# Kernel tuning notes

Hardware: AMD Instinct MI355X
Metric: run time of the kernel (lower is better)

Reference implementation:

```python
import jax, jax.numpy as jnp
import numpy as np

EPS = 1e-3  # Keras BatchNormalization default epsilon


def _bn_params(key, c):
    k1, k2, k3, k4 = jax.random.split(key, 4)
    gamma = 1.0 + 0.1 * jax.random.normal(k1, (c,), jnp.float32)
    beta = 0.1 * jax.random.normal(k2, (c,), jnp.float32)
    mean = 0.1 * jax.random.normal(k3, (c,), jnp.float32)
    var = 0.5 + jax.random.uniform(k4, (c,), jnp.float32)
    return jnp.stack([gamma, beta, mean, var])  # (4, c)


def bn(x, p):
    g, b, m, v = p[0], p[1], p[2], p[3]
    return (x - m) * jax.lax.rsqrt(v + EPS) * g + b


def setup_inputs() -> dict:
    key = jax.random.key(0)
    ks = jax.random.split(key, 32)
    B, N, C, K = 32, 2048, 3, 32
    MLP1, UNITS = 128, 512
    w = lambda k, shp, fan: jax.random.normal(k, shp, jnp.float32) / np.sqrt(fan)
    inp = {
        "inputs": jax.random.normal(ks[0], (B, N, C), jnp.float32),
        "indices": jax.random.randint(ks[1], (B, N, K), 0, N, jnp.int32),
        "t_conv1_w": w(ks[2], (C, 64), C), "t_conv1_b": 0.1 * jax.random.normal(ks[3], (64,), jnp.float32),
        "t_bn1": _bn_params(ks[4], 64),
        "t_dense1_w": w(ks[5], (64, 64), 64), "t_dense1_b": 0.1 * jax.random.normal(ks[6], (64,), jnp.float32),
        "t_bn2": _bn_params(ks[7], 64),
        "t_dense2_w": w(ks[8], (64, C * C), 64), "t_dense2_b": 0.1 * jax.random.normal(ks[9], (C * C,), jnp.float32),
        "conv1_w": w(ks[10], (K * C, MLP1), K * C), "conv1_b": 0.1 * jax.random.normal(ks[11], (MLP1,), jnp.float32),
        "bn1": _bn_params(ks[12], MLP1),
        "conv2_w": w(ks[13], (MLP1, 2 * MLP1), MLP1), "conv2_b": 0.1 * jax.random.normal(ks[14], (2 * MLP1,), jnp.float32),
        "bn2": _bn_params(ks[15], 2 * MLP1),
        "bn3": _bn_params(ks[16], 2 * MLP1),
        "dense1_w": w(ks[17], (2 * MLP1, C), 2 * MLP1), "dense1_b": 0.1 * jax.random.normal(ks[18], (C,), jnp.float32),
        "conv3_w": w(ks[19], (C, UNITS), C), "conv3_b": 0.1 * jax.random.normal(ks[20], (UNITS,), jnp.float32),
        "bn4": _bn_params(ks[21], UNITS),
        "blk1_w": w(ks[22], (UNITS, UNITS // 2), UNITS), "blk1_b": 0.1 * jax.random.normal(ks[23], (UNITS // 2,), jnp.float32),
        "blk1_bn": _bn_params(ks[24], UNITS // 2),
        "blk2_w": w(ks[25], (UNITS // 2, UNITS // 4), UNITS // 2), "blk2_b": 0.1 * jax.random.normal(ks[26], (UNITS // 4,), jnp.float32),
        "blk2_bn": _bn_params(ks[27], UNITS // 4),
        "bn_globf": _bn_params(ks[28], UNITS // 4),
    }
    return inp


def reference(inputs, indices, t_conv1_w, t_conv1_b, t_bn1, t_dense1_w, t_dense1_b,
              t_bn2, t_dense2_w, t_dense2_b, conv1_w, conv1_b, bn1, conv2_w, conv2_b,
              bn2, bn3, dense1_w, dense1_b, conv3_w, conv3_b, bn4,
              blk1_w, blk1_b, blk1_bn, blk2_w, blk2_b, blk2_bn, bn_globf):
    B, N, C = inputs.shape
    # --- TNetLess (inference: dropout = identity) ---
    x = jax.nn.relu(bn(inputs @ t_conv1_w + t_conv1_b, t_bn1))   # (B,N,64)
    x = jnp.max(x, axis=1)                                        # global max pool -> (B,64)
    x = jax.nn.relu(bn(x @ t_dense1_w + t_dense1_b, t_bn2))      # (B,64)
    transform = (x @ t_dense2_w + t_dense2_b).reshape(B, C, C)   # (B,C,C)
    pct = jnp.einsum('bnc,bcd->bnd', inputs, transform)          # transformed cloud (B,N,C)
    # --- random neighbor gather (batch_dims=1) ---
    feats = pct[jnp.arange(B)[:, None, None], indices]           # (B,N,K,C)
    feats = feats.reshape(B, N, -1)                               # (B,N,K*C)
    # --- pointwise MLP over gathered neighbor features ---
    feats = jax.nn.relu(bn(feats @ conv1_w + conv1_b, bn1))      # (B,N,128)
    feats = jax.nn.relu(bn(feats @ conv2_w + conv2_b, bn2))      # (B,N,256)
    g = bn(jnp.max(feats, axis=1), bn3)                           # (B,256)
    g = jnp.broadcast_to(g[:, None, :], (B, N, g.shape[-1]))     # tile to (B,N,256)
    g = g @ dense1_w + dense1_b                                   # (B,N,C)
    combined = jnp.concatenate([pct, g], axis=1)                  # concat on point axis -> (B,2N,C)
    # --- conv3 + conv blocks (kernel_size=1 -> pointwise) ---
    net = jax.nn.relu(bn(combined @ conv3_w + conv3_b, bn4))     # (B,2N,512)
    net = jax.nn.relu(bn(net @ blk1_w + blk1_b, blk1_bn))        # (B,2N,256)
    net = jax.nn.relu(bn(net @ blk2_w + blk2_b, blk2_bn))        # (B,2N,128)
    net = jnp.max(net, axis=1)                                    # (B,128)
    return bn(net, bn_globf)
```

## Files before the change

### kernel.cpp

```cpp
#include <hip/hip_runtime.h>

typedef unsigned short u16;
typedef unsigned int u32;
typedef __attribute__((ext_vector_type(8))) short bf16x8;
typedef __attribute__((ext_vector_type(4))) float f32x4;

#define EPSBN 0.001f
#define MFMA16(a, b, c) __builtin_amdgcn_mfma_f32_16x16x32_bf16(a, b, c, 0, 0, 0)

__device__ __forceinline__ float bf2f(u16 u) {
    return __uint_as_float(((u32)u) << 16);
}
__device__ __forceinline__ u16 f2bf(float f) {
    u32 u = __float_as_uint(f);
    u32 r = u + 0x7FFFu + ((u >> 16) & 1u);
    return (u16)(r >> 16);
}
__device__ __forceinline__ float relu(float x) { return x > 0.f ? x : 0.f; }

#define A_INPUTS 64
#define A_TC1W  196672
#define A_TC1B  196864
#define A_TBN1  196928
#define A_TD1W  197184
#define A_TD1B  201280
#define A_TBN2  201344
#define A_TD2W  201600
#define A_TD2B  202176
#define A_C1W   202240
#define A_C1B   214528
#define A_BN1   214656
#define A_C2W   215168
#define A_C2B   247936
#define A_BN2   248192
#define A_BN3   249216
#define A_D1W   250240
#define A_D1B   251008
#define A_C3W   251072
#define A_C3B   252608
#define A_BN4   253120
#define A_BLK1W 255168
#define A_BLK1B 386240
#define A_BLK1BN 386496
#define A_BLK2W 387520
#define A_BLK2B 420288
#define A_BLK2BN 420416
#define A_BNGF  420928
#define S_TRF   423488
#define S_PCT   423808
#define S_MAXF  620544
#define S_NETMAX 628736
#define S_XMAX  632832
#define T_C1WT  634880
#define T_C2WT  641024
#define T_W4T   657408
#define T_W5T   722944
#define P_W3S   739328
#define P_B3S   740864
#define P_BP1   741376
#define P_BP2   741504
#define P_BP4   741760
#define P_BP5   742016

struct ConvArgs {
    const void* src[28];
    int n[28];
    int off[28];
};

struct PrepArgs {
    const float* src[4];
    const float* bn[4];
    u16* dst[4];
    int K[4];
    int logN[4];
    int base[4];
};

__global__ __launch_bounds__(256) void k_convert(ConvArgs a, const u16* __restrict__ tbn1,
                                                 float* __restrict__ ws, u32* __restrict__ flag) {
    int ok = 1;
    for (int i = 0; i < 16; i += 2) {
        u16 v = tbn1[i];
        if (v < 0x3E00u || v > 0x4080u) ok = 0;
    }
    if (blockIdx.x == 0 && blockIdx.y == 0 && threadIdx.x == 0) flag[0] = ok ? 1u : 0u;

    int t = blockIdx.y;
    int n = a.n[t];
    int cpb = (n + 31) >> 5;
    int s = blockIdx.x * cpb;
    int e = s + cpb; if (e > n) e = n;
    float* dst = ws + a.off[t];
    if (ok) {
        const u16* src = (const u16*)a.src[t];
        for (int i = s + (int)threadIdx.x; i < e; i += 256) dst[i] = bf2f(src[i]);
    } else {
        const float* src = (const float*)a.src[t];
        for (int i = s + (int)threadIdx.x; i < e; i += 256) dst[i] = src[i];
    }
}

__global__ __launch_bounds__(256) void k_prepw_all(PrepArgs pa) {
    int blk = blockIdx.x;
    int t = (blk < 48) ? 0 : (blk < 176) ? 1 : (blk < 688) ? 2 : 3;
    int i = (blk - pa.base[t]) * 256 + (int)threadIdx.x;
    int N = 1 << pa.logN[t];
    int k = i >> pa.logN[t], c = i & (N - 1);
    const float* bn = pa.bn[t];
    float s = bn[c] * rsqrtf(bn[3 * N + c] + EPSBN);
    pa.dst[t][c * pa.K[t] + k] = f2bf(pa.src[t][i] * s);
}

__global__ __launch_bounds__(256) void k_prepsmall(float* __restrict__ ws) {
    int tid = threadIdx.x;
    for (int c = tid; c < 512; c += 256) {
        const float* bn = ws + A_BN4;
        float s = bn[c] * rsqrtf(bn[1536 + c] + EPSBN);
        float t = bn[512 + c] - bn[1024 + c] * s;
        ws[P_W3S + c]        = ws[A_C3W + c] * s;
        ws[P_W3S + 512 + c]  = ws[A_C3W + 512 + c] * s;
        ws[P_W3S + 1024 + c] = ws[A_C3W + 1024 + c] * s;
        ws[P_B3S + c] = ws[A_C3B + c] * s + t;
    }
    {
        int c = tid;
        const float* bn2 = ws + A_BN2;
        float s2 = bn2[c] * rsqrtf(bn2[768 + c] + EPSBN);
        ws[P_BP2 + c] = ws[A_C2B + c] * s2 + (bn2[256 + c] - bn2[512 + c] * s2);
        const float* bn5 = ws + A_BLK1BN;
        float s5 = bn5[c] * rsqrtf(bn5[768 + c] + EPSBN);
        ws[P_BP4 + c] = ws[A_BLK1B + c] * s5 + (bn5[256 + c] - bn5[512 + c] * s5);
    }
    if (tid < 128) {
        int c = tid;
        const float* bn1 = ws + A_BN1;
        float s1 = bn1[c] * rsqrtf(bn1[384 + c] + EPSBN);
        ws[P_BP1 + c] = ws[A_C1B + c] * s1 + (bn1[128 + c] - bn1[256 + c] * s1);
        const float* bn6 = ws + A_BLK2BN;
        float s6 = bn6[c] * rsqrtf(bn6[384 + c] + EPSBN);
        ws[P_BP5 + c] = ws[A_BLK2B + c] * s6 + (bn6[128 + c] - bn6[256 + c] * s6);
    }
}

__global__ __launch_bounds__(256) void k_tnet1(const float* __restrict__ inp,
                                               const float* __restrict__ w,
                                               const float* __restrict__ bias,
                                               const float* __restrict__ bn,
                                               u32* __restrict__ xmax) {
    __shared__ float pts[1536];
    __shared__ float wred[4][64];
    int b = blockIdx.y, slice = blockIdx.x, tid = threadIdx.x;
    const float* ip = inp + ((size_t)b * 2048 + slice * 512) * 3;
#pragma unroll
    for (int i = 0; i < 6; i++) pts[tid + i * 256] = ip[tid + i * 256];

    int c = tid & 63, np = tid >> 6;
    float w0 = w[c], w1 = w[64 + c], w2 = w[128 + c], bi = bias[c];
    float g = bn[c], be = bn[64 + c], m = bn[128 + c], v = bn[192 + c];
    float s = g * rsqrtf(v + EPSBN), t = be - m * s;
    __syncthreads();

    float vmax = 0.f;
    int pbase = np * 128;
#pragma unroll 4
    for (int p = 0; p < 128; p++) {
        float x0 = pts[(pbase + p) * 3], x1 = pts[(pbase + p) * 3 + 1], x2 = pts[(pbase + p) * 3 + 2];
        float z = x0 * w0 + x1 * w1 + x2 * w2 + bi;
        vmax = fmaxf(vmax, z * s + t);
    }
    wred[np][c] = vmax;
    __syncthreads();
    if (tid < 64) {
        float mm = fmaxf(fmaxf(wred[0][tid], wred[1][tid]), fmaxf(wred[2][tid], wred[3][tid]));
        atomicMax(&xmax[b * 64 + tid], __float_as_uint(relu(mm)));
    }
}

__global__ __launch_bounds__(64) void k_tnet2(const float* __restrict__ xmax,
                                              const float* __restrict__ w1, const float* __restrict__ b1,
                                              const float* __restrict__ bn2p,
                                              const float* __restrict__ w2, const float* __restrict__ b2,
                                              float* __restrict__ transform) {
    int b = blockIdx.x, t = threadIdx.x;
    __shared__ float x2[64];
    const float* xm = xmax + b * 64;
    float acc = b1[t];
    for (int j = 0; j < 64; j++) acc += xm[j] * w1[j * 64 + t];
    float g = bn2p[t], be = bn2p[64 + t], m = bn2p[128 + t], v = bn2p[192 + t];
    float s = g * rsqrtf(v + EPSBN);
    x2[t] = relu(acc * s + (be - m * s));
    __syncthreads();
    if (t < 9) {
        float a = b2[t];
        for (int j = 0; j < 64; j++) a += x2[j] * w2[j * 9 + t];
        transform[b * 9 + t] = a;
    }
}

__global__ __launch_bounds__(256) void k_pct(const float* __restrict__ inp,
                                             const float* __restrict__ transform,
                                             float* __restrict__ pct) {
    int b = blockIdx.y;
    int n = blockIdx.x * 256 + threadIdx.x;
    __shared__ float T[9];
    if (threadIdx.x < 9) T[threadIdx.x] = transform[b * 9 + threadIdx.x];
    __syncthreads();
    const float* ip = inp + ((size_t)b * 2048 + n) * 3;
    float x0 = ip[0], x1 = ip[1], x2 = ip[2];
    float* op = pct + ((size_t)b * 2049 + n) * 3;
    op[0] = x0 * T[0] + x1 * T[3] + x2 * T[6];
    op[1] = x0 * T[1] + x1 * T[4] + x2 * T[7];
    op[2] = x0 * T[2] + x1 * T[5] + x2 * T[8];
}

__global__ __launch_bounds__(256, 3) void k_feat(const float* __restrict__ pct,
                                                 const int* __restrict__ indices,
                                                 const u16* __restrict__ w1t, const float* __restrict__ bp1,
                                                 const u16* __restrict__ w2t, const float* __restrict__ bp2,
                                                 u32* __restrict__ maxfeats) {
    __shared__ __align__(16) u16 ftA[8192];
    __shared__ __align__(16) u16 h1B[8192];
    __shared__ float sp1[128], sp2[256];

    int b = blockIdx.y, n0p = blockIdx.x * 64, tid = threadIdx.x;
    sp2[tid] = bp2[tid];
    if (tid < 128) sp1[tid] = bp1[tid];
    {
        const float* pb = pct + (size_t)b * 2049 * 3;
        const int* ib = indices + ((size_t)b * 2048 + n0p) * 32;
        char* fA = (char*)ftA;
#pragma unroll
        for (int r = 0; r < 8; r++) {
            int i = tid + 256 * r;
            int p = i >> 5, k = i & 31;
            int idx = ib[p * 32 + k];
            const float* s = pb + (size_t)idx * 3;
            int sw = (p & 7) << 4;
            int base = p * 256 + 6 * k;
            *(u16*)(fA + ((base) ^ sw))     = f2bf(s[0]);
            *(u16*)(fA + ((base + 2) ^ sw)) = f2bf(s[1]);
            *(u16*)(fA + ((base + 4) ^ sw)) = f2bf(s[2]);
        }
    }
    __syncthreads();

    int lane = tid & 63, wv = tid >> 6;
    int rw = lane & 15, kq = lane >> 4;
    int axor = (rw & 7) << 4;

    {
        f32x4 acc[4][2];
#pragma unroll
        for (int m = 0; m < 4; m++)
#pragma unroll
            for (int n = 0; n < 2; n++) acc[m][n] = (f32x4){0.f, 0.f, 0.f, 0.f};
        const char* A = (const char*)ftA;
        const char* W = (const char*)w1t;
        int nb = wv * 32;
#pragma unroll
        for (int ks = 0; ks < 3; ks++) {
            int kb = ks * 64 + kq * 16;
            bf16x8 b0 = *(const bf16x8*)(W + (nb + rw) * 192 + kb);
            bf16x8 b1 = *(const bf16x8*)(W + (nb + 16 + rw) * 192 + kb);
            bf16x8 a0 = *(const bf16x8*)(A + (((rw) * 256 + kb) ^ axor));
            bf16x8 a1 = *(const bf16x8*)(A + (((rw + 16) * 256 + kb) ^ axor));
            bf16x8 a2 = *(const bf16x8*)(A + (((rw + 32) * 256 + kb) ^ axor));
            bf16x8 a3 = *(const bf16x8*)(A + (((rw + 48) * 256 + kb) ^ axor));
            acc[0][0] = MFMA16(a0, b0, acc[0][0]); acc[0][1] = MFMA16(a0, b1, acc[0][1]);
            acc[1][0] = MFMA16(a1, b0, acc[1][0]); acc[1][1] = MFMA16(a1, b1, acc[1][1]);
            acc[2][0] = MFMA16(a2, b0, acc[2][0]); acc[2][1] = MFMA16(a2, b1, acc[2][1]);
            acc[3][0] = MFMA16(a3, b0, acc[3][0]); acc[3][1] = MFMA16(a3, b1, acc[3][1]);
        }
        char* hB = (char*)h1B;
#pragma unroll
        for (int nt = 0; nt < 2; nt++) {
            int c = nb + nt * 16 + rw;
            float bb = sp1[c];
#pragma unroll
            for (int m = 0; m < 4; m++)
#pragma unroll
                for (int r = 0; r < 4; r++) {
                    int rr = m * 16 + kq * 4 + r;
                    float h = relu(acc[m][nt][r] + bb);
                    *(u16*)(hB + ((rr * 256 + c * 2) ^ ((rr & 7) << 4))) = f2bf(h);
                }
        }
    }
    __syncthreads();
    {
        f32x4 acc[4][4];
#pragma unroll
        for (int m = 0; m < 4; m++)
#pragma unroll
            for (int n = 0; n < 4; n++) acc[m][n] = (f32x4){0.f, 0.f, 0.f, 0.f};
        const char* A = (const char*)h1B;
        const char* W = (const char*)w2t;
        int nb = wv * 64;
#pragma unroll
        for (int ks = 0; ks < 4; ks++) {
            int kb = ks * 64 + kq * 16;
            bf16x8 a0 = *(const bf16x8*)(A + (((rw) * 256 + kb) ^ axor));
            bf16x8 a1 = *(const bf16x8*)(A + (((rw + 16) * 256 + kb) ^ axor));
            bf16x8 a2 = *(const bf16x8*)(A + (((rw + 32) * 256 + kb) ^ axor));
            bf16x8 a3 = *(const bf16x8*)(A + (((rw + 48) * 256 + kb) ^ axor));
#pragma unroll
            for (int nt = 0; nt < 4; nt++) {
                bf16x8 bv = *(const bf16x8*)(W + (nb + nt * 16 + rw) * 256 + kb);
                acc[0][nt] = MFMA16(a0, bv, acc[0][nt]);
                acc[1][nt] = MFMA16(a1, bv, acc[1][nt]);
                acc[2][nt] = MFMA16(a2, bv, acc[2][nt]);
                acc[3][nt] = MFMA16(a3, bv, acc[3][nt]);
            }
        }
#pragma unroll
        for (int nt = 0; nt < 4; nt++) {
            int c = nb + nt * 16 + rw;
            float bb = sp2[c];
            float vm = 0.f;
#pragma unroll
            for (int m = 0; m < 4; m++)
#pragma unroll
                for (int r = 0; r < 4; r++)
                    vm = fmaxf(vm, relu(acc[m][nt][r] + bb));
            vm = fmaxf(vm, __shfl_xor(vm, 16));
            vm = fmaxf(vm, __shfl_xor(vm, 32));
            if (kq == 0) atomicMax(&maxfeats[b * 256 + c], __float_as_uint(vm));
        }
    }
}

__global__ __launch_bounds__(256) void k_gvec(const u32* __restrict__ maxfeats,
                                              const float* __restrict__ bn3p,
                                              const float* __restrict__ dw, const float* __restrict__ db,
                                              float* __restrict__ pct) {
    int b = blockIdx.x, c = threadIdx.x;
    __shared__ float red[3][256];
    float mf = __uint_as_float(maxfeats[b * 256 + c]);
    float g = bn3p[c], be = bn3p[256 + c], m = bn3p[512 + c], v = bn3p[768 + c];
    float s = g * rsqrtf(v + EPSBN);
    float y = mf * s + (be - m * s);
    red[0][c] = y * dw[c * 3 + 0];
    red[1][c] = y * dw[c * 3 + 1];
    red[2][c] = y * dw[c * 3 + 2];
    __syncthreads();
    for (int st = 128; st > 0; st >>= 1) {
        if (c < st) {
            red[0][c] += red[0][c + st];
            red[1][c] += red[1][c + st];
            red[2][c] += red[2][c + st];
        }
        __syncthreads();
    }
    if (c < 3) pct[((size_t)b * 2049 + 2048) * 3 + c] = red[c][0] + db[c];
}

__global__ __launch_bounds__(256, 3) void k_mlp(const float* __restrict__ pct,
                                                const float* __restrict__ w3s, const float* __restrict__ b3s,
                                                const u16* __restrict__ w4t, const float* __restrict__ bp4,
                                                const u16* __restrict__ w5t, const float* __restrict__ bp5,
                                                u32* __restrict__ netmax) {
    __shared__ __align__(16) u16 hA[2][4096];
    __shared__ __align__(16) u16 hB[16384];
    __shared__ float rows4[256];
    __shared__ float sb4[256], sb5[128];

    int b = blockIdx.y, r0 = blockIdx.x * 64, tid = threadIdx.x;
    int nrows = 2049 - r0; if (nrows > 64) nrows = 64;

    sb4[tid] = bp4[tid];
    if (tid < 128) sb5[tid] = bp5[tid];
    if (tid < 64) {
        float v0 = 0.f, v1 = 0.f, v2 = 0.f;
        if (tid < nrows) {
            const float* s = pct + ((size_t)b * 2049 + r0 + tid) * 3;
            v0 = s[0]; v1 = s[1]; v2 = s[2];
        }
        rows4[tid * 4] = v0; rows4[tid * 4 + 1] = v1; rows4[tid * 4 + 2] = v2;
    }
    __syncthreads();

    int lane = tid & 63, wv = tid >> 6;
    int rw = lane & 15, kq = lane >> 4;
    int axor = (rw & 7) << 4;
    int chv = tid & 63;
    int rquart = tid >> 6;

    auto phase1 = [&](int c, int bufi) {
        int ch = c * 64 + chv;
        float w0 = w3s[ch], w1 = w3s[512 + ch], w2 = w3s[1024 + ch], bb = b3s[ch];
        char* dst = (char*)hA[bufi];
#pragma unroll
        for (int r = 0; r < 16; r++) {
            int row = rquart * 16 + r;
            float x0 = rows4[row * 4], x1 = rows4[row * 4 + 1], x2 = rows4[row * 4 + 2];
            float h = relu(x0 * w0 + x1 * w1 + x2 * w2 + bb);
            *(u16*)(dst + ((row * 128 + chv * 2) ^ ((row & 7) << 4))) = f2bf(h);
        }
    };

    phase1(0, 0);
    __syncthreads();

    {
        f32x4 acc[4][4];
#pragma unroll
        for (int m = 0; m < 4; m++)
#pragma unroll
            for (int n = 0; n < 4; n++) acc[m][n] = (f32x4){0.f, 0.f, 0.f, 0.f};
        const char* W = (const char*)w4t;
        int nb = wv * 64;
        for (int c = 0; c < 8; c++) {
            bf16x8 bfr[2][4];
#pragma unroll
            for (int ksl = 0; ksl < 2; ksl++)
#pragma unroll
                for (int nt = 0; nt < 4; nt++)
                    bfr[ksl][nt] = *(const bf16x8*)(W + (nb + nt * 16 + rw) * 1024 + c * 128 + ksl * 64 + kq * 16);
            if (c < 7) phase1(c + 1, (c + 1) & 1);
            const char* A = (const char*)hA[c & 1];
#pragma unroll
            for (int ksl = 0; ksl < 2; ksl++) {
                int kb = ksl * 64 + kq * 16;
                bf16x8 a0 = *(const bf16x8*)(A + (((rw) * 128 + kb) ^ axor));
                bf16x8 a1 = *(const bf16x8*)(A + (((rw + 16) * 128 + kb) ^ axor));
                bf16x8 a2 = *(const bf16x8*)(A + (((rw + 32) * 128 + kb) ^ axor));
                bf16x8 a3 = *(const bf16x8*)(A + (((rw + 48) * 128 + kb) ^ axor));
#pragma unroll
                for (int nt = 0; nt < 4; nt++) {
                    acc[0][nt] = MFMA16(a0, bfr[ksl][nt], acc[0][nt]);
                    acc[1][nt] = MFMA16(a1, bfr[ksl][nt], acc[1][nt]);
                    acc[2][nt] = MFMA16(a2, bfr[ksl][nt], acc[2][nt]);
                    acc[3][nt] = MFMA16(a3, bfr[ksl][nt], acc[3][nt]);
                }
            }
            __syncthreads();
        }
        char* HB = (char*)hB;
#pragma unroll
        for (int nt = 0; nt < 4; nt++) {
            int c = nb + nt * 16 + rw;
            float bb = sb4[c];
#pragma unroll
            for (int m = 0; m < 4; m++)
#pragma unroll
                for (int r = 0; r < 4; r++) {
                    int rr = m * 16 + kq * 4 + r;
                    float h = relu(acc[m][nt][r] + bb);
                    *(u16*)(HB + ((rr * 512 + c * 2) ^ ((rr & 7) << 4))) = f2bf(h);
                }
        }
    }
    __syncthreads();
    {
        f32x4 acc[4][2];
#pragma unroll
        for (int m = 0; m < 4; m++)
#pragma unroll
            for (int n = 0; n < 2; n++) acc[m][n] = (f32x4){0.f, 0.f, 0.f, 0.f};
        const char* A = (const char*)hB;
        const char* W = (const char*)w5t;
        int nb = wv * 32;
#pragma unroll
        for (int ks = 0; ks < 8; ks++) {
            int kb = ks * 64 + kq * 16;
            bf16x8 b0 = *(const bf16x8*)(W + (nb + rw) * 512 + kb);
            bf16x8 b1 = *(const bf16x8*)(W + (nb + 16 + rw) * 512 + kb);
            bf16x8 a0 = *(const bf16x8*)(A + (((rw) * 512 + kb) ^ axor));
            bf16x8 a1 = *(const bf16x8*)(A + (((rw + 16) * 512 + kb) ^ axor));
            bf16x8 a2 = *(const bf16x8*)(A + (((rw + 32) * 512 + kb) ^ axor));
            bf16x8 a3 = *(const bf16x8*)(A + (((rw + 48) * 512 + kb) ^ axor));
            acc[0][0] = MFMA16(a0, b0, acc[0][0]); acc[0][1] = MFMA16(a0, b1, acc[0][1]);
            acc[1][0] = MFMA16(a1, b0, acc[1][0]); acc[1][1] = MFMA16(a1, b1, acc[1][1]);
            acc[2][0] = MFMA16(a2, b0, acc[2][0]); acc[2][1] = MFMA16(a2, b1, acc[2][1]);
            acc[3][0] = MFMA16(a3, b0, acc[3][0]); acc[3][1] = MFMA16(a3, b1, acc[3][1]);
        }
#pragma unroll
        for (int nt = 0; nt < 2; nt++) {
            int c = nb + nt * 16 + rw;
            float bb = sb5[c];
            float vm = 0.f;
#pragma unroll
            for (int m = 0; m < 4; m++)
#pragma unroll
                for (int r = 0; r < 4; r++) {
                    int rr = m * 16 + kq * 4 + r;
                    float h = relu(acc[m][nt][r] + bb);
                    if (rr < nrows) vm = fmaxf(vm, h);
                }
            vm = fmaxf(vm, __shfl_xor(vm, 16));
            vm = fmaxf(vm, __shfl_xor(vm, 32));
            if (kq == 0) atomicMax(&netmax[b * 128 + c], __float_as_uint(vm));
        }
    }
}

__global__ __launch_bounds__(256) void k_out(const u32* __restrict__ netmax,
                                             const float* __restrict__ bng,
                                             const u32* __restrict__ flag,
                                             void* __restrict__ out) {
    int i = blockIdx.x * 256 + threadIdx.x;
    int c = i & 127;
    float v = __uint_as_float(netmax[i]);
    float g = bng[c], be = bng[128 + c], m = bng[256 + c], va = bng[384 + c];
    float s = g * rsqrtf(va + EPSBN);
    float val = v * s + (be - m * s);
    if (flag[0]) ((u16*)out)[i] = f2bf(val);
    else ((float*)out)[i] = val;
}

extern "C" void kernel_launch(void* const* d_in, const int* in_sizes, int n_in,
                              void* d_out, int out_size, void* d_ws, size_t ws_size,
                              hipStream_t stream) {
    float* ws = (float*)d_ws;
    u32* flag = (u32*)ws;

    static const int order[28] = {0,2,3,4,5,6,7,8,9,10,11,12,13,14,15,16,17,18,19,20,21,22,23,24,25,26,27,28};
    static const int nels[28] = {196608,192,64,256,4096,64,256,576,9,12288,128,512,32768,256,1024,1024,768,3,1536,512,2048,131072,256,1024,32768,128,512,512};
    static const int offs[28] = {A_INPUTS,A_TC1W,A_TC1B,A_TBN1,A_TD1W,A_TD1B,A_TBN2,A_TD2W,A_TD2B,A_C1W,A_C1B,A_BN1,A_C2W,A_C2B,A_BN2,A_BN3,A_D1W,A_D1B,A_C3W,A_C3B,A_BN4,A_BLK1W,A_BLK1B,A_BLK1BN,A_BLK2W,A_BLK2B,A_BLK2BN,A_BNGF};
    ConvArgs ca;
    for (int i = 0; i < 28; i++) { ca.src[i] = d_in[order[i]]; ca.n[i] = nels[i]; ca.off[i] = offs[i]; }

    const int* indices = (const int*)d_in[1];

    k_convert<<<dim3(32, 28), 256, 0, stream>>>(ca, (const u16*)d_in[4], ws, flag);

    PrepArgs pa;
    pa.src[0] = ws + A_C1W;   pa.bn[0] = ws + A_BN1;    pa.dst[0] = (u16*)(ws + T_C1WT); pa.K[0] = 96;  pa.logN[0] = 7; pa.base[0] = 0;
    pa.src[1] = ws + A_C2W;   pa.bn[1] = ws + A_BN2;    pa.dst[1] = (u16*)(ws + T_C2WT); pa.K[1] = 128; pa.logN[1] = 8; pa.base[1] = 48;
    pa.src[2] = ws + A_BLK1W; pa.bn[2] = ws + A_BLK1BN; pa.dst[2] = (u16*)(ws + T_W4T);  pa.K[2] = 512; pa.logN[2] = 8; pa.base[2] = 176;
    pa.src[3] = ws + A_BLK2W; pa.bn[3] = ws + A_BLK2BN; pa.dst[3] = (u16*)(ws + T_W5T);  pa.K[3] = 256; pa.logN[3] = 7; pa.base[3] = 688;
    k_prepw_all<<<816, 256, 0, stream>>>(pa);
    k_prepsmall<<<1, 256, 0, stream>>>(ws);

    hipMemsetAsync(ws + S_MAXF, 0, (size_t)14336 * 4, stream);

    k_tnet1<<<dim3(4, 32), 256, 0, stream>>>(ws + A_INPUTS, ws + A_TC1W, ws + A_TC1B, ws + A_TBN1,
                                             (u32*)(ws + S_XMAX));
    k_tnet2<<<32, 64, 0, stream>>>((const float*)(ws + S_XMAX), ws + A_TD1W, ws + A_TD1B, ws + A_TBN2,
                                   ws + A_TD2W, ws + A_TD2B, ws + S_TRF);
    k_pct<<<dim3(8, 32), 256, 0, stream>>>(ws + A_INPUTS, ws + S_TRF, ws + S_PCT);
    k_feat<<<dim3(32, 32), 256, 0, stream>>>(ws + S_PCT, indices,
                                             (const u16*)(ws + T_C1WT), ws + P_BP1,
                                             (const u16*)(ws + T_C2WT), ws + P_BP2,
                                             (u32*)(ws + S_MAXF));
    k_gvec<<<32, 256, 0, stream>>>((u32*)(ws + S_MAXF), ws + A_BN3, ws + A_D1W, ws + A_D1B, ws + S_PCT);
    k_mlp<<<dim3(33, 32), 256, 0, stream>>>(ws + S_PCT,
                                            ws + P_W3S, ws + P_B3S,
                                            (const u16*)(ws + T_W4T), ws + P_BP4,
                                            (const u16*)(ws + T_W5T), ws + P_BP5,
                                            (u32*)(ws + S_NETMAX));
    k_out<<<16, 256, 0, stream>>>((u32*)(ws + S_NETMAX), ws + A_BNGF, flag, d_out);
}
```

Measured before the change: 223.8 us.

## Merge prep kernels, fuse T-Net stages, and co-schedule feature and MLP passes

Collapses the convert, weight-prep, small-prep and memset launches into one prep kernel. That kernel reads raw inputs with a runtime bf16/f32 test and writes folded weights straight to workspace, skipping the full fp32 staging copy. The two T-Net kernels become one block per batch. The neighbor-feature MLP and the point MLP become a single launch with interleaved blocks, and the global-vector rows move into a small tail kernel. The aim is fewer launches and less intermediate traffic, at the cost of more complex branching and heavier per-block T-Net work.

```diff
diff --git a/kernel.cpp b/kernel.cpp
--- a/kernel.cpp
+++ b/kernel.cpp
@@ -17,6 +17,9 @@
     return (u16)(r >> 16);
 }
 __device__ __forceinline__ float relu(float x) { return x > 0.f ? x : 0.f; }
+__device__ __forceinline__ float rdv(const void* p, int i, int isbf) {
+    return isbf ? bf2f(((const u16*)p)[i]) : ((const float*)p)[i];
+}
 
 #define A_INPUTS 64
 #define A_TC1W  196672
@@ -27,30 +30,14 @@
 #define A_TBN2  201344
 #define A_TD2W  201600
 #define A_TD2B  202176
-#define A_C1W   202240
-#define A_C1B   214528
-#define A_BN1   214656
-#define A_C2W   215168
-#define A_C2B   247936
-#define A_BN2   248192
 #define A_BN3   249216
 #define A_D1W   250240
 #define A_D1B   251008
-#define A_C3W   251072
-#define A_C3B   252608
-#define A_BN4   253120
-#define A_BLK1W 255168
-#define A_BLK1B 386240
-#define A_BLK1BN 386496
-#define A_BLK2W 387520
-#define A_BLK2B 420288
-#define A_BLK2BN 420416
 #define A_BNGF  420928
 #define S_TRF   423488
 #define S_PCT   423808
 #define S_MAXF  620544
 #define S_NETMAX 628736
-#define S_XMAX  632832
 #define T_C1WT  634880
 #define T_C2WT  641024
 #define T_W4T   657408
@@ -62,139 +49,118 @@
 #define P_BP4   741760
 #define P_BP5   742016
 
-struct ConvArgs {
-    const void* src[28];
-    int n[28];
-    int off[28];
-};
-
-struct PrepArgs {
-    const float* src[4];
-    const float* bn[4];
-    u16* dst[4];
-    int K[4];
-    int logN[4];
-    int base[4];
-};
-
-__global__ __launch_bounds__(256) void k_convert(ConvArgs a, const u16* __restrict__ tbn1,
-                                                 float* __restrict__ ws, u32* __restrict__ flag) {
-    int ok = 1;
+struct SmallCv { const void* src[12]; int n[12]; int off[12]; };
+struct PrepWA { const void* src[4]; const void* bn[4]; int K[4]; int logN[4]; int base[4]; int dstoff[4]; };
+struct PrepSm { const void *bn4, *c3w, *c3b, *bn2, *c2b, *blk1bn, *blk1b, *bn1, *c1b, *blk2bn, *blk2b; };
+
+__global__ __launch_bounds__(256) void k_prep(SmallCv sc, PrepWA pw, PrepSm ps,
+                                              const void* __restrict__ inputs_raw,
+                                              const u16* __restrict__ tbn1_raw,
+                                              float* __restrict__ ws) {
+    int isbf = 1;
     for (int i = 0; i < 16; i += 2) {
-        u16 v = tbn1[i];
-        if (v < 0x3E00u || v > 0x4080u) ok = 0;
-    }
-    if (blockIdx.x == 0 && blockIdx.y == 0 && threadIdx.x == 0) flag[0] = ok ? 1u : 0u;
-
-    int t = blockIdx.y;
-    int n = a.n[t];
-    int cpb = (n + 31) >> 5;
-    int s = blockIdx.x * cpb;
-    int e = s + cpb; if (e > n) e = n;
-    float* dst = ws + a.off[t];
-    if (ok) {
-        const u16* src = (const u16*)a.src[t];
-        for (int i = s + (int)threadIdx.x; i < e; i += 256) dst[i] = bf2f(src[i]);
+        u16 v = tbn1_raw[i];
+        if (v < 0x3E00u || v > 0x4080u) isbf = 0;
+    }
+    int bx = blockIdx.x, tid = threadIdx.x;
+    if (bx < 32) {
+        float* dst = ws + A_INPUTS;
+        for (int i = bx * 256 + tid; i < 196608; i += 8192) dst[i] = rdv(inputs_raw, i, isbf);
+    } else if (bx < 36) {
+        int t0 = (bx - 32) * 3;
+        for (int t = t0; t < t0 + 3; t++) {
+            int n = sc.n[t];
+            float* dst = ws + sc.off[t];
+            for (int i = tid; i < n; i += 256) dst[i] = rdv(sc.src[t], i, isbf);
+        }
+    } else if (bx < 852) {
+        int blk = bx - 36;
+        int t = (blk < 48) ? 0 : (blk < 176) ? 1 : (blk < 688) ? 2 : 3;
+        int i = (blk - pw.base[t]) * 256 + tid;
+        int N = 1 << pw.logN[t];
+        int k = i >> pw.logN[t], c = i & (N - 1);
+        float s = rdv(pw.bn[t], c, isbf) * rsqrtf(rdv(pw.bn[t], 3 * N + c, isbf) + EPSBN);
+        ((u16*)(ws + pw.dstoff[t]))[c * pw.K[t] + k] = f2bf(rdv(pw.src[t], i, isbf) * s);
+    } else if (bx == 852) {
+        for (int c = tid; c < 512; c += 256) {
+            float s = rdv(ps.bn4, c, isbf) * rsqrtf(rdv(ps.bn4, 1536 + c, isbf) + EPSBN);
+            float t = rdv(ps.bn4, 512 + c, isbf) - rdv(ps.bn4, 1024 + c, isbf) * s;
+            ws[P_W3S + c]        = rdv(ps.c3w, c, isbf) * s;
+            ws[P_W3S + 512 + c]  = rdv(ps.c3w, 512 + c, isbf) * s;
+            ws[P_W3S + 1024 + c] = rdv(ps.c3w, 1024 + c, isbf) * s;
+            ws[P_B3S + c] = rdv(ps.c3b, c, isbf) * s + t;
+        }
+        {
+            int c = tid;
+            float s2 = rdv(ps.bn2, c, isbf) * rsqrtf(rdv(ps.bn2, 768 + c, isbf) + EPSBN);
+            ws[P_BP2 + c] = rdv(ps.c2b, c, isbf) * s2 + (rdv(ps.bn2, 256 + c, isbf) - rdv(ps.bn2, 512 + c, isbf) * s2);
+            float s5 = rdv(ps.blk1bn, c, isbf) * rsqrtf(rdv(ps.blk1bn, 768 + c, isbf) + EPSBN);
+            ws[P_BP4 + c] = rdv(ps.blk1b, c, isbf) * s5 + (rdv(ps.blk1bn, 256 + c, isbf) - rdv(ps.blk1bn, 512 + c, isbf) * s5);
+        }
+        if (tid < 128) {
+            int c = tid;
+            float s1 = rdv(ps.bn1, c, isbf) * rsqrtf(rdv(ps.bn1, 384 + c, isbf) + EPSBN);
+            ws[P_BP1 + c] = rdv(ps.c1b, c, isbf) * s1 + (rdv(ps.bn1, 128 + c, isbf) - rdv(ps.bn1, 256 + c, isbf) * s1);
+            float s6 = rdv(ps.blk2bn, c, isbf) * rsqrtf(rdv(ps.blk2bn, 384 + c, isbf) + EPSBN);
+            ws[P_BP5 + c] = rdv(ps.blk2b, c, isbf) * s6 + (rdv(ps.blk2bn, 128 + c, isbf) - rdv(ps.blk2bn, 256 + c, isbf) * s6);
+        }
     } else {
-        const float* src = (const float*)a.src[t];
-        for (int i = s + (int)threadIdx.x; i < e; i += 256) dst[i] = src[i];
-    }
-}
-
-__global__ __launch_bounds__(256) void k_prepw_all(PrepArgs pa) {
-    int blk = blockIdx.x;
-    int t = (blk < 48) ? 0 : (blk < 176) ? 1 : (blk < 688) ? 2 : 3;
-    int i = (blk - pa.base[t]) * 256 + (int)threadIdx.x;
-    int N = 1 << pa.logN[t];
-    int k = i >> pa.logN[t], c = i & (N - 1);
-    const float* bn = pa.bn[t];
-    float s = bn[c] * rsqrtf(bn[3 * N + c] + EPSBN);
-    pa.dst[t][c * pa.K[t] + k] = f2bf(pa.src[t][i] * s);
-}
-
-__global__ __launch_bounds__(256) void k_prepsmall(float* __restrict__ ws) {
-    int tid = threadIdx.x;
-    for (int c = tid; c < 512; c += 256) {
-        const float* bn = ws + A_BN4;
-        float s = bn[c] * rsqrtf(bn[1536 + c] + EPSBN);
-        float t = bn[512 + c] - bn[1024 + c] * s;
-        ws[P_W3S + c]        = ws[A_C3W + c] * s;
-        ws[P_W3S + 512 + c]  = ws[A_C3W + 512 + c] * s;
-        ws[P_W3S + 1024 + c] = ws[A_C3W + 1024 + c] * s;
-        ws[P_B3S + c] = ws[A_C3B + c] * s + t;
-    }
-    {
-        int c = tid;
-        const float* bn2 = ws + A_BN2;
-        float s2 = bn2[c] * rsqrtf(bn2[768 + c] + EPSBN);
-        ws[P_BP2 + c] = ws[A_C2B + c] * s2 + (bn2[256 + c] - bn2[512 + c] * s2);
-        const float* bn5 = ws + A_BLK1BN;
-        float s5 = bn5[c] * rsqrtf(bn5[768 + c] + EPSBN);
-        ws[P_BP4 + c] = ws[A_BLK1B + c] * s5 + (bn5[256 + c] - bn5[512 + c] * s5);
-    }
-    if (tid < 128) {
-        int c = tid;
-        const float* bn1 = ws + A_BN1;
-        float s1 = bn1[c] * rsqrtf(bn1[384 + c] + EPSBN);
-        ws[P_BP1 + c] = ws[A_C1B + c] * s1 + (bn1[128 + c] - bn1[256 + c] * s1);
-        const float* bn6 = ws + A_BLK2BN;
-        float s6 = bn6[c] * rsqrtf(bn6[384 + c] + EPSBN);
-        ws[P_BP5 + c] = ws[A_BLK2B + c] * s6 + (bn6[128 + c] - bn6[256 + c] * s6);
-    }
-}
-
-__global__ __launch_bounds__(256) void k_tnet1(const float* __restrict__ inp,
-                                               const float* __restrict__ w,
-                                               const float* __restrict__ bias,
-                                               const float* __restrict__ bn,
-                                               u32* __restrict__ xmax) {
-    __shared__ float pts[1536];
-    __shared__ float wred[4][64];
-    int b = blockIdx.y, slice = blockIdx.x, tid = threadIdx.x;
-    const float* ip = inp + ((size_t)b * 2048 + slice * 512) * 3;
-#pragma unroll
-    for (int i = 0; i < 6; i++) pts[tid + i * 256] = ip[tid + i * 256];
-
-    int c = tid & 63, np = tid >> 6;
-    float w0 = w[c], w1 = w[64 + c], w2 = w[128 + c], bi = bias[c];
-    float g = bn[c], be = bn[64 + c], m = bn[128 + c], v = bn[192 + c];
-    float s = g * rsqrtf(v + EPSBN), t = be - m * s;
-    __syncthreads();
-
-    float vmax = 0.f;
-    int pbase = np * 128;
-#pragma unroll 4
-    for (int p = 0; p < 128; p++) {
-        float x0 = pts[(pbase + p) * 3], x1 = pts[(pbase + p) * 3 + 1], x2 = pts[(pbase + p) * 3 + 2];
-        float z = x0 * w0 + x1 * w1 + x2 * w2 + bi;
-        vmax = fmaxf(vmax, z * s + t);
-    }
-    wred[np][c] = vmax;
-    __syncthreads();
-    if (tid < 64) {
-        float mm = fmaxf(fmaxf(wred[0][tid], wred[1][tid]), fmaxf(wred[2][tid], wred[3][tid]));
-        atomicMax(&xmax[b * 64 + tid], __float_as_uint(relu(mm)));
-    }
-}
-
-__global__ __launch_bounds__(64) void k_tnet2(const float* __restrict__ xmax,
+        u32* z = (u32*)(ws + S_MAXF);
+        for (int i = tid; i < 12288; i += 256) z[i] = 0u;
+        if (tid == 0) ((u32*)ws)[0] = (u32)isbf;
+    }
+}
+
+__global__ __launch_bounds__(256) void k_tnet(const float* __restrict__ inp,
+                                              const float* __restrict__ w,
+                                              const float* __restrict__ bias,
+                                              const float* __restrict__ bn,
                                               const float* __restrict__ w1, const float* __restrict__ b1,
                                               const float* __restrict__ bn2p,
                                               const float* __restrict__ w2, const float* __restrict__ b2,
                                               float* __restrict__ transform) {
-    int b = blockIdx.x, t = threadIdx.x;
-    __shared__ float x2[64];
-    const float* xm = xmax + b * 64;
-    float acc = b1[t];
-    for (int j = 0; j < 64; j++) acc += xm[j] * w1[j * 64 + t];
-    float g = bn2p[t], be = bn2p[64 + t], m = bn2p[128 + t], v = bn2p[192 + t];
-    float s = g * rsqrtf(v + EPSBN);
-    x2[t] = relu(acc * s + (be - m * s));
-    __syncthreads();
-    if (t < 9) {
-        float a = b2[t];
-        for (int j = 0; j < 64; j++) a += x2[j] * w2[j * 9 + t];
-        transform[b * 9 + t] = a;
+    __shared__ float pts[6144];
+    __shared__ float wred[4][64];
+    __shared__ float x1v[64];
+    __shared__ float x2v[64];
+    int b = blockIdx.x, tid = threadIdx.x;
+    const float* ip = inp + (size_t)b * 2048 * 3;
+#pragma unroll
+    for (int i = 0; i < 24; i++) pts[tid + i * 256] = ip[tid + i * 256];
+
+    int c = tid & 63, pg = tid >> 6;
+    float w0 = w[c], w1c = w[64 + c], w2c = w[128 + c], bi = bias[c];
+    float g = bn[c], be = bn[64 + c], m = bn[128 + c], v = bn[192 + c];
+    float s = g * rsqrtf(v + EPSBN), t = be - m * s;
+    __syncthreads();
+
+    float vmax = 0.f;
+    int pbase = pg * 512;
+#pragma unroll 4
+    for (int p = 0; p < 512; p++) {
+        float x0 = pts[(pbase + p) * 3], x1 = pts[(pbase + p) * 3 + 1], x2 = pts[(pbase + p) * 3 + 2];
+        float z = x0 * w0 + x1 * w1c + x2 * w2c + bi;
+        vmax = fmaxf(vmax, z * s + t);
+    }
+    wred[pg][c] = vmax;
+    __syncthreads();
+    if (tid < 64) {
+        float mm = fmaxf(fmaxf(wred[0][tid], wred[1][tid]), fmaxf(wred[2][tid], wred[3][tid]));
+        x1v[tid] = relu(mm);
+    }
+    __syncthreads();
+    if (tid < 64) {
+        float acc = b1[tid];
+        for (int j = 0; j < 64; j++) acc += x1v[j] * w1[j * 64 + tid];
+        float g2 = bn2p[tid], be2 = bn2p[64 + tid], m2 = bn2p[128 + tid], v2 = bn2p[192 + tid];
+        float s2 = g2 * rsqrtf(v2 + EPSBN);
+        x2v[tid] = relu(acc * s2 + (be2 - m2 * s2));
+    }
+    __syncthreads();
+    if (tid < 9) {
+        float a = b2[tid];
+        for (int j = 0; j < 64; j++) a += x2v[j] * w2[j * 9 + tid];
+        transform[b * 9 + tid] = a;
     }
 }
 
@@ -208,134 +174,269 @@
     __syncthreads();
     const float* ip = inp + ((size_t)b * 2048 + n) * 3;
     float x0 = ip[0], x1 = ip[1], x2 = ip[2];
-    float* op = pct + ((size_t)b * 2049 + n) * 3;
+    float* op = pct + ((size_t)b * 2048 + n) * 3;
     op[0] = x0 * T[0] + x1 * T[3] + x2 * T[6];
     op[1] = x0 * T[1] + x1 * T[4] + x2 * T[7];
     op[2] = x0 * T[2] + x1 * T[5] + x2 * T[8];
 }
 
-__global__ __launch_bounds__(256, 3) void k_feat(const float* __restrict__ pct,
-                                                 const int* __restrict__ indices,
-                                                 const u16* __restrict__ w1t, const float* __restrict__ bp1,
-                                                 const u16* __restrict__ w2t, const float* __restrict__ bp2,
-                                                 u32* __restrict__ maxfeats) {
-    __shared__ __align__(16) u16 ftA[8192];
-    __shared__ __align__(16) u16 h1B[8192];
-    __shared__ float sp1[128], sp2[256];
-
-    int b = blockIdx.y, n0p = blockIdx.x * 64, tid = threadIdx.x;
-    sp2[tid] = bp2[tid];
-    if (tid < 128) sp1[tid] = bp1[tid];
-    {
-        const float* pb = pct + (size_t)b * 2049 * 3;
-        const int* ib = indices + ((size_t)b * 2048 + n0p) * 32;
-        char* fA = (char*)ftA;
-#pragma unroll
-        for (int r = 0; r < 8; r++) {
-            int i = tid + 256 * r;
-            int p = i >> 5, k = i & 31;
-            int idx = ib[p * 32 + k];
-            const float* s = pb + (size_t)idx * 3;
-            int sw = (p & 7) << 4;
-            int base = p * 256 + 6 * k;
-            *(u16*)(fA + ((base) ^ sw))     = f2bf(s[0]);
-            *(u16*)(fA + ((base + 2) ^ sw)) = f2bf(s[1]);
-            *(u16*)(fA + ((base + 4) ^ sw)) = f2bf(s[2]);
-        }
-    }
-    __syncthreads();
-
+__global__ __launch_bounds__(256, 3) void k_featmlp(
+    const float* __restrict__ pct, const int* __restrict__ indices,
+    const u16* __restrict__ w1t, const float* __restrict__ bp1,
+    const u16* __restrict__ w2t, const float* __restrict__ bp2,
+    u32* __restrict__ maxfeats,
+    const float* __restrict__ w3s, const float* __restrict__ b3s,
+    const u16* __restrict__ w4t, const float* __restrict__ bp4,
+    const u16* __restrict__ w5t, const float* __restrict__ bp5,
+    u32* __restrict__ netmax) {
+    __shared__ __align__(16) char SM[51712];
+    int bx = blockIdx.x, tid = threadIdx.x;
+    int part = bx & 1;
+    int idx = bx >> 1;
+    int b = idx >> 5, sub = idx & 31;
     int lane = tid & 63, wv = tid >> 6;
     int rw = lane & 15, kq = lane >> 4;
     int axor = (rw & 7) << 4;
 
-    {
-        f32x4 acc[4][2];
-#pragma unroll
-        for (int m = 0; m < 4; m++)
-#pragma unroll
-            for (int n = 0; n < 2; n++) acc[m][n] = (f32x4){0.f, 0.f, 0.f, 0.f};
-        const char* A = (const char*)ftA;
-        const char* W = (const char*)w1t;
-        int nb = wv * 32;
-#pragma unroll
-        for (int ks = 0; ks < 3; ks++) {
-            int kb = ks * 64 + kq * 16;
-            bf16x8 b0 = *(const bf16x8*)(W + (nb + rw) * 192 + kb);
-            bf16x8 b1 = *(const bf16x8*)(W + (nb + 16 + rw) * 192 + kb);
-            bf16x8 a0 = *(const bf16x8*)(A + (((rw) * 256 + kb) ^ axor));
-            bf16x8 a1 = *(const bf16x8*)(A + (((rw + 16) * 256 + kb) ^ axor));
-            bf16x8 a2 = *(const bf16x8*)(A + (((rw + 32) * 256 + kb) ^ axor));
-            bf16x8 a3 = *(const bf16x8*)(A + (((rw + 48) * 256 + kb) ^ axor));
-            acc[0][0] = MFMA16(a0, b0, acc[0][0]); acc[0][1] = MFMA16(a0, b1, acc[0][1]);
-            acc[1][0] = MFMA16(a1, b0, acc[1][0]); acc[1][1] = MFMA16(a1, b1, acc[1][1]);
-            acc[2][0] = MFMA16(a2, b0, acc[2][0]); acc[2][1] = MFMA16(a2, b1, acc[2][1]);
-            acc[3][0] = MFMA16(a3, b0, acc[3][0]); acc[3][1] = MFMA16(a3, b1, acc[3][1]);
-        }
-        char* hB = (char*)h1B;
-#pragma unroll
-        for (int nt = 0; nt < 2; nt++) {
-            int c = nb + nt * 16 + rw;
-            float bb = sp1[c];
+    if (part == 0) {
+        char* ftA = SM;
+        char* h1B = SM + 16384;
+        float* sp1 = (float*)(SM + 32768);
+        float* sp2 = (float*)(SM + 33280);
+        int n0p = sub * 64;
+        sp2[tid] = bp2[tid];
+        if (tid < 128) sp1[tid] = bp1[tid];
+        {
+            const float* pb = pct + (size_t)b * 2048 * 3;
+            const int* ib = indices + ((size_t)b * 2048 + n0p) * 32;
+#pragma unroll
+            for (int r = 0; r < 8; r++) {
+                int i = tid + 256 * r;
+                int p = i >> 5, k = i & 31;
+                int idxp = ib[p * 32 + k];
+                const float* s = pb + (size_t)idxp * 3;
+                int sw = (p & 7) << 4;
+                int base = p * 256 + 6 * k;
+                *(u16*)(ftA + ((base) ^ sw))     = f2bf(s[0]);
+                *(u16*)(ftA + ((base + 2) ^ sw)) = f2bf(s[1]);
+                *(u16*)(ftA + ((base + 4) ^ sw)) = f2bf(s[2]);
+            }
+        }
+        __syncthreads();
+        {
+            f32x4 acc[4][2];
 #pragma unroll
             for (int m = 0; m < 4; m++)
 #pragma unroll
-                for (int r = 0; r < 4; r++) {
-                    int rr = m * 16 + kq * 4 + r;
-                    float h = relu(acc[m][nt][r] + bb);
-                    *(u16*)(hB + ((rr * 256 + c * 2) ^ ((rr & 7) << 4))) = f2bf(h);
+                for (int n = 0; n < 2; n++) acc[m][n] = (f32x4){0.f, 0.f, 0.f, 0.f};
+            const char* W = (const char*)w1t;
+            int nb = wv * 32;
+#pragma unroll
+            for (int ks = 0; ks < 3; ks++) {
+                int kb = ks * 64 + kq * 16;
+                bf16x8 b0 = *(const bf16x8*)(W + (nb + rw) * 192 + kb);
+                bf16x8 b1 = *(const bf16x8*)(W + (nb + 16 + rw) * 192 + kb);
+                bf16x8 a0 = *(const bf16x8*)(ftA + (((rw) * 256 + kb) ^ axor));
+                bf16x8 a1 = *(const bf16x8*)(ftA + (((rw + 16) * 256 + kb) ^ axor));
+                bf16x8 a2 = *(const bf16x8*)(ftA + (((rw + 32) * 256 + kb) ^ axor));
+                bf16x8 a3 = *(const bf16x8*)(ftA + (((rw + 48) * 256 + kb) ^ axor));
+                acc[0][0] = MFMA16(a0, b0, acc[0][0]); acc[0][1] = MFMA16(a0, b1, acc[0][1]);
+                acc[1][0] = MFMA16(a1, b0, acc[1][0]); acc[1][1] = MFMA16(a1, b1, acc[1][1]);
+                acc[2][0] = MFMA16(a2, b0, acc[2][0]); acc[2][1] = MFMA16(a2, b1, acc[2][1]);
+                acc[3][0] = MFMA16(a3, b0, acc[3][0]); acc[3][1] = MFMA16(a3, b1, acc[3][1]);
+            }
+#pragma unroll
+            for (int nt = 0; nt < 2; nt++) {
+                int c = nb + nt * 16 + rw;
+                float bb = sp1[c];
+#pragma unroll
+                for (int m = 0; m < 4; m++)
+#pragma unroll
+                    for (int r = 0; r < 4; r++) {
+                        int rr = m * 16 + kq * 4 + r;
+                        float h = relu(acc[m][nt][r] + bb);
+                        *(u16*)(h1B + ((rr * 256 + c * 2) ^ ((rr & 7) << 4))) = f2bf(h);
+                    }
+            }
+        }
+        __syncthreads();
+        {
+            f32x4 acc[4][4];
+#pragma unroll
+            for (int m = 0; m < 4; m++)
+#pragma unroll
+                for (int n = 0; n < 4; n++) acc[m][n] = (f32x4){0.f, 0.f, 0.f, 0.f};
+            const char* W = (const char*)w2t;
+            int nb = wv * 64;
+#pragma unroll
+            for (int ks = 0; ks < 4; ks++) {
+                int kb = ks * 64 + kq * 16;
+                bf16x8 a0 = *(const bf16x8*)(h1B + (((rw) * 256 + kb) ^ axor));
+                bf16x8 a1 = *(const bf16x8*)(h1B + (((rw + 16) * 256 + kb) ^ axor));
+                bf16x8 a2 = *(const bf16x8*)(h1B + (((rw + 32) * 256 + kb) ^ axor));
+                bf16x8 a3 = *(const bf16x8*)(h1B + (((rw + 48) * 256 + kb) ^ axor));
+#pragma unroll
+                for (int nt = 0; nt < 4; nt++) {
+                    bf16x8 bv = *(const bf16x8*)(W + (nb + nt * 16 + rw) * 256 + kb);
+                    acc[0][nt] = MFMA16(a0, bv, acc[0][nt]);
+                    acc[1][nt] = MFMA16(a1, bv, acc[1][nt]);
+                    acc[2][nt] = MFMA16(a2, bv, acc[2][nt]);
+                    acc[3][nt] = MFMA16(a3, bv, acc[3][nt]);
                 }
-        }
-    }
-    __syncthreads();
-    {
-        f32x4 acc[4][4];
-#pragma unroll
-        for (int m = 0; m < 4; m++)
-#pragma unroll
-            for (int n = 0; n < 4; n++) acc[m][n] = (f32x4){0.f, 0.f, 0.f, 0.f};
-        const char* A = (const char*)h1B;
-        const char* W = (const char*)w2t;
-        int nb = wv * 64;
-#pragma unroll
-        for (int ks = 0; ks < 4; ks++) {
-            int kb = ks * 64 + kq * 16;
-            bf16x8 a0 = *(const bf16x8*)(A + (((rw) * 256 + kb) ^ axor));
-            bf16x8 a1 = *(const bf16x8*)(A + (((rw + 16) * 256 + kb) ^ axor));
-            bf16x8 a2 = *(const bf16x8*)(A + (((rw + 32) * 256 + kb) ^ axor));
-            bf16x8 a3 = *(const bf16x8*)(A + (((rw + 48) * 256 + kb) ^ axor));
+            }
 #pragma unroll
             for (int nt = 0; nt < 4; nt++) {
-                bf16x8 bv = *(const bf16x8*)(W + (nb + nt * 16 + rw) * 256 + kb);
-                acc[0][nt] = MFMA16(a0, bv, acc[0][nt]);
-                acc[1][nt] = MFMA16(a1, bv, acc[1][nt]);
-                acc[2][nt] = MFMA16(a2, bv, acc[2][nt]);
-                acc[3][nt] = MFMA16(a3, bv, acc[3][nt]);
-            }
-        }
-#pragma unroll
-        for (int nt = 0; nt < 4; nt++) {
-            int c = nb + nt * 16 + rw;
-            float bb = sp2[c];
-            float vm = 0.f;
+                int c = nb + nt * 16 + rw;
+                float bb = sp2[c];
+                float vm = 0.f;
+#pragma unroll
+                for (int m = 0; m < 4; m++)
+#pragma unroll
+                    for (int r = 0; r < 4; r++)
+                        vm = fmaxf(vm, relu(acc[m][nt][r] + bb));
+                vm = fmaxf(vm, __shfl_xor(vm, 16));
+                vm = fmaxf(vm, __shfl_xor(vm, 32));
+                if (kq == 0) atomicMax(&maxfeats[b * 256 + c], __float_as_uint(vm));
+            }
+        }
+    } else {
+        char* hA0 = SM;
+        char* hA1 = SM + 8192;
+        char* HB  = SM + 16384;
+        float* rows4 = (float*)(SM + 49152);
+        float* sb4 = (float*)(SM + 50176);
+        float* sb5 = (float*)(SM + 51200);
+        int r0 = sub * 64;
+
+        sb4[tid] = bp4[tid];
+        if (tid < 128) sb5[tid] = bp5[tid];
+        if (tid < 64) {
+            const float* s = pct + ((size_t)b * 2048 + r0 + tid) * 3;
+            rows4[tid * 4] = s[0]; rows4[tid * 4 + 1] = s[1]; rows4[tid * 4 + 2] = s[2];
+        }
+        __syncthreads();
+
+        auto phase1 = [&](int c, char* dst) {
+            int c2 = (tid & 31) * 2;
+            int rg = tid >> 5;
+            int ch = c * 64 + c2;
+            float wa0 = w3s[ch], wa1 = w3s[512 + ch], wa2 = w3s[1024 + ch], ba = b3s[ch];
+            float wb0 = w3s[ch + 1], wb1 = w3s[513 + ch], wb2 = w3s[1025 + ch], bb2 = b3s[ch + 1];
+#pragma unroll
+            for (int r = 0; r < 8; r++) {
+                int row = rg * 8 + r;
+                float x0 = rows4[row * 4], x1 = rows4[row * 4 + 1], x2 = rows4[row * 4 + 2];
+                float ha = relu(x0 * wa0 + x1 * wa1 + x2 * wa2 + ba);
+                float hb = relu(x0 * wb0 + x1 * wb1 + x2 * wb2 + bb2);
+                u32 pk = (u32)f2bf(ha) | ((u32)f2bf(hb) << 16);
+                *(u32*)(dst + ((row * 128 + c2 * 2) ^ ((row & 7) << 4))) = pk;
+            }
+        };
+
+        phase1(0, hA0);
+        __syncthreads();
+
+        {
+            f32x4 acc[4][4];
 #pragma unroll
             for (int m = 0; m < 4; m++)
 #pragma unroll
-                for (int r = 0; r < 4; r++)
-                    vm = fmaxf(vm, relu(acc[m][nt][r] + bb));
-            vm = fmaxf(vm, __shfl_xor(vm, 16));
-            vm = fmaxf(vm, __shfl_xor(vm, 32));
-            if (kq == 0) atomicMax(&maxfeats[b * 256 + c], __float_as_uint(vm));
-        }
-    }
-}
-
-__global__ __launch_bounds__(256) void k_gvec(const u32* __restrict__ maxfeats,
-                                              const float* __restrict__ bn3p,
-                                              const float* __restrict__ dw, const float* __restrict__ db,
-                                              float* __restrict__ pct) {
+                for (int n = 0; n < 4; n++) acc[m][n] = (f32x4){0.f, 0.f, 0.f, 0.f};
+            const char* W = (const char*)w4t;
+            int nb = wv * 64;
+            for (int c = 0; c < 8; c++) {
+                bf16x8 bfr[2][4];
+#pragma unroll
+                for (int ksl = 0; ksl < 2; ksl++)
+#pragma unroll
+                    for (int nt = 0; nt < 4; nt++)
+                        bfr[ksl][nt] = *(const bf16x8*)(W + (nb + nt * 16 + rw) * 1024 + c * 128 + ksl * 64 + kq * 16);
+                if (c < 7) phase1(c + 1, (c & 1) ? hA0 : hA1);
+                const char* A = (c & 1) ? hA1 : hA0;
+#pragma unroll
+                for (int ksl = 0; ksl < 2; ksl++) {
+                    int kb = ksl * 64 + kq * 16;
+                    bf16x8 a0 = *(const bf16x8*)(A + (((rw) * 128 + kb) ^ axor));
+                    bf16x8 a1 = *(const bf16x8*)(A + (((rw + 16) * 128 + kb) ^ axor));
+                    bf16x8 a2 = *(const bf16x8*)(A + (((rw + 32) * 128 + kb) ^ axor));
+                    bf16x8 a3 = *(const bf16x8*)(A + (((rw + 48) * 128 + kb) ^ axor));
+#pragma unroll
+                    for (int nt = 0; nt < 4; nt++) {
+                        acc[0][nt] = MFMA16(a0, bfr[ksl][nt], acc[0][nt]);
+                        acc[1][nt] = MFMA16(a1, bfr[ksl][nt], acc[1][nt]);
+                        acc[2][nt] = MFMA16(a2, bfr[ksl][nt], acc[2][nt]);
+                        acc[3][nt] = MFMA16(a3, bfr[ksl][nt], acc[3][nt]);
+                    }
+                }
+                __syncthreads();
+            }
+#pragma unroll
+            for (int nt = 0; nt < 4; nt++) {
+                int c = nb + nt * 16 + rw;
+                float bb = sb4[c];
+#pragma unroll
+                for (int m = 0; m < 4; m++)
+#pragma unroll
+                    for (int r = 0; r < 4; r++) {
+                        int rr = m * 16 + kq * 4 + r;
+                        float h = relu(acc[m][nt][r] + bb);
+                        *(u16*)(HB + ((rr * 512 + c * 2) ^ ((rr & 7) << 4))) = f2bf(h);
+                    }
+            }
+        }
+        __syncthreads();
+        {
+            f32x4 acc[4][2];
+#pragma unroll
+            for (int m = 0; m < 4; m++)
+#pragma unroll
+                for (int n = 0; n < 2; n++) acc[m][n] = (f32x4){0.f, 0.f, 0.f, 0.f};
+            const char* W = (const char*)w5t;
+            int nb = wv * 32;
+#pragma unroll
+            for (int ks = 0; ks < 8; ks++) {
+                int kb = ks * 64 + kq * 16;
+                bf16x8 b0 = *(const bf16x8*)(W + (nb + rw) * 512 + kb);
+                bf16x8 b1 = *(const bf16x8*)(W + (nb + 16 + rw) * 512 + kb);
+                bf16x8 a0 = *(const bf16x8*)(HB + (((rw) * 512 + kb) ^ axor));
+                bf16x8 a1 = *(const bf16x8*)(HB + (((rw + 16) * 512 + kb) ^ axor));
+                bf16x8 a2 = *(const bf16x8*)(HB + (((rw + 32) * 512 + kb) ^ axor));
+                bf16x8 a3 = *(const bf16x8*)(HB + (((rw + 48) * 512 + kb) ^ axor));
+                acc[0][0] = MFMA16(a0, b0, acc[0][0]); acc[0][1] = MFMA16(a0, b1, acc[0][1]);
+                acc[1][0] = MFMA16(a1, b0, acc[1][0]); acc[1][1] = MFMA16(a1, b1, acc[1][1]);
+                acc[2][0] = MFMA16(a2, b0, acc[2][0]); acc[2][1] = MFMA16(a2, b1, acc[2][1]);
+                acc[3][0] = MFMA16(a3, b0, acc[3][0]); acc[3][1] = MFMA16(a3, b1, acc[3][1]);
+            }
+#pragma unroll
+            for (int nt = 0; nt < 2; nt++) {
+                int c = nb + nt * 16 + rw;
+                float bb = sb5[c];
+                float vm = 0.f;
+#pragma unroll
+                for (int m = 0; m < 4; m++)
+#pragma unroll
+                    for (int r = 0; r < 4; r++)
+                        vm = fmaxf(vm, relu(acc[m][nt][r] + bb));
+                vm = fmaxf(vm, __shfl_xor(vm, 16));
+                vm = fmaxf(vm, __shfl_xor(vm, 32));
+                if (kq == 0) atomicMax(&netmax[b * 128 + c], __float_as_uint(vm));
+            }
+        }
+    }
+}
+
+__global__ __launch_bounds__(256) void k_gtail(const u32* __restrict__ maxfeats,
+                                               const float* __restrict__ bn3p,
+                                               const float* __restrict__ dw, const float* __restrict__ db,
+                                               const float* __restrict__ w3s, const float* __restrict__ b3s,
+                                               const u16* __restrict__ w4t, const float* __restrict__ bp4,
+                                               const u16* __restrict__ w5t, const float* __restrict__ bp5,
+                                               u32* __restrict__ netmax) {
+    __shared__ float red[3][256];
+    __shared__ float h512[512];
+    __shared__ float h256[256];
+    __shared__ float gv[4];
     int b = blockIdx.x, c = threadIdx.x;
-    __shared__ float red[3][256];
     float mf = __uint_as_float(maxfeats[b * 256 + c]);
     float g = bn3p[c], be = bn3p[256 + c], m = bn3p[512 + c], v = bn3p[768 + c];
     float s = g * rsqrtf(v + EPSBN);
@@ -352,146 +453,32 @@
         }
         __syncthreads();
     }
-    if (c < 3) pct[((size_t)b * 2049 + 2048) * 3 + c] = red[c][0] + db[c];
-}
-
-__global__ __launch_bounds__(256, 3) void k_mlp(const float* __restrict__ pct,
-                                                const float* __restrict__ w3s, const float* __restrict__ b3s,
-                                                const u16* __restrict__ w4t, const float* __restrict__ bp4,
-                                                const u16* __restrict__ w5t, const float* __restrict__ bp5,
-                                                u32* __restrict__ netmax) {
-    __shared__ __align__(16) u16 hA[2][4096];
-    __shared__ __align__(16) u16 hB[16384];
-    __shared__ float rows4[256];
-    __shared__ float sb4[256], sb5[128];
-
-    int b = blockIdx.y, r0 = blockIdx.x * 64, tid = threadIdx.x;
-    int nrows = 2049 - r0; if (nrows > 64) nrows = 64;
-
-    sb4[tid] = bp4[tid];
-    if (tid < 128) sb5[tid] = bp5[tid];
-    if (tid < 64) {
-        float v0 = 0.f, v1 = 0.f, v2 = 0.f;
-        if (tid < nrows) {
-            const float* s = pct + ((size_t)b * 2049 + r0 + tid) * 3;
-            v0 = s[0]; v1 = s[1]; v2 = s[2];
-        }
-        rows4[tid * 4] = v0; rows4[tid * 4 + 1] = v1; rows4[tid * 4 + 2] = v2;
-    }
-    __syncthreads();
-
-    int lane = tid & 63, wv = tid >> 6;
-    int rw = lane & 15, kq = lane >> 4;
-    int axor = (rw & 7) << 4;
-    int chv = tid & 63;
-    int rquart = tid >> 6;
-
-    auto phase1 = [&](int c, int bufi) {
-        int ch = c * 64 + chv;
-        float w0 = w3s[ch], w1 = w3s[512 + ch], w2 = w3s[1024 + ch], bb = b3s[ch];
-        char* dst = (char*)hA[bufi];
-#pragma unroll
-        for (int r = 0; r < 16; r++) {
-            int row = rquart * 16 + r;
-            float x0 = rows4[row * 4], x1 = rows4[row * 4 + 1], x2 = rows4[row * 4 + 2];
-            float h = relu(x0 * w0 + x1 * w1 + x2 * w2 + bb);
-            *(u16*)(dst + ((row * 128 + chv * 2) ^ ((row & 7) << 4))) = f2bf(h);
-        }
-    };
-
-    phase1(0, 0);
-    __syncthreads();
-
+    if (c < 3) gv[c] = red[c][0] + db[c];
+    __syncthreads();
+    float g0 = gv[0], g1 = gv[1], g2 = gv[2];
+    for (int h = c; h < 512; h += 256)
+        h512[h] = relu(g0 * w3s[h] + g1 * w3s[512 + h] + g2 * w3s[1024 + h] + b3s[h]);
+    __syncthreads();
     {
-        f32x4 acc[4][4];
-#pragma unroll
-        for (int m = 0; m < 4; m++)
-#pragma unroll
-            for (int n = 0; n < 4; n++) acc[m][n] = (f32x4){0.f, 0.f, 0.f, 0.f};
-        const char* W = (const char*)w4t;
-        int nb = wv * 64;
-        for (int c = 0; c < 8; c++) {
-            bf16x8 bfr[2][4];
-#pragma unroll
-            for (int ksl = 0; ksl < 2; ksl++)
-#pragma unroll
-                for (int nt = 0; nt < 4; nt++)
-                    bfr[ksl][nt] = *(const bf16x8*)(W + (nb + nt * 16 + rw) * 1024 + c * 128 + ksl * 64 + kq * 16);
-            if (c < 7) phase1(c + 1, (c + 1) & 1);
-            const char* A = (const char*)hA[c & 1];
-#pragma unroll
-            for (int ksl = 0; ksl < 2; ksl++) {
-                int kb = ksl * 64 + kq * 16;
-                bf16x8 a0 = *(const bf16x8*)(A + (((rw) * 128 + kb) ^ axor));
-                bf16x8 a1 = *(const bf16x8*)(A + (((rw + 16) * 128 + kb) ^ axor));
-                bf16x8 a2 = *(const bf16x8*)(A + (((rw + 32) * 128 + kb) ^ axor));
-                bf16x8 a3 = *(const bf16x8*)(A + (((rw + 48) * 128 + kb) ^ axor));
-#pragma unroll
-                for (int nt = 0; nt < 4; nt++) {
-                    acc[0][nt] = MFMA16(a0, bfr[ksl][nt], acc[0][nt]);
-                    acc[1][nt] = MFMA16(a1, bfr[ksl][nt], acc[1][nt]);
-                    acc[2][nt] = MFMA16(a2, bfr[ksl][nt], acc[2][nt]);
-                    acc[3][nt] = MFMA16(a3, bfr[ksl][nt], acc[3][nt]);
-                }
-            }
-            __syncthreads();
-        }
-        char* HB = (char*)hB;
-#pragma unroll
-        for (int nt = 0; nt < 4; nt++) {
-            int c = nb + nt * 16 + rw;
-            float bb = sb4[c];
-#pragma unroll
-            for (int m = 0; m < 4; m++)
-#pragma unroll
-                for (int r = 0; r < 4; r++) {
-                    int rr = m * 16 + kq * 4 + r;
-                    float h = relu(acc[m][nt][r] + bb);
-                    *(u16*)(HB + ((rr * 512 + c * 2) ^ ((rr & 7) << 4))) = f2bf(h);
-                }
-        }
-    }
-    __syncthreads();
-    {
-        f32x4 acc[4][2];
-#pragma unroll
-        for (int m = 0; m < 4; m++)
-#pragma unroll
-            for (int n = 0; n < 2; n++) acc[m][n] = (f32x4){0.f, 0.f, 0.f, 0.f};
-        const char* A = (const char*)hB;
-        const char* W = (const char*)w5t;
-        int nb = wv * 32;
-#pragma unroll
-        for (int ks = 0; ks < 8; ks++) {
-            int kb = ks * 64 + kq * 16;
-            bf16x8 b0 = *(const bf16x8*)(W + (nb + rw) * 512 + kb);
-            bf16x8 b1 = *(const bf16x8*)(W + (nb + 16 + rw) * 512 + kb);
-            bf16x8 a0 = *(const bf16x8*)(A + (((rw) * 512 + kb) ^ axor));
-            bf16x8 a1 = *(const bf16x8*)(A + (((rw + 16) * 512 + kb) ^ axor));
-            bf16x8 a2 = *(const bf16x8*)(A + (((rw + 32) * 512 + kb) ^ axor));
-            bf16x8 a3 = *(const bf16x8*)(A + (((rw + 48) * 512 + kb) ^ axor));
-            acc[0][0] = MFMA16(a0, b0, acc[0][0]); acc[0][1] = MFMA16(a0, b1, acc[0][1]);
-            acc[1][0] = MFMA16(a1, b0, acc[1][0]); acc[1][1] = MFMA16(a1, b1, acc[1][1]);
-            acc[2][0] = MFMA16(a2, b0, acc[2][0]); acc[2][1] = MFMA16(a2, b1, acc[2][1]);
-            acc[3][0] = MFMA16(a3, b0, acc[3][0]); acc[3][1] = MFMA16(a3, b1, acc[3][1]);
-        }
-#pragma unroll
-        for (int nt = 0; nt < 2; nt++) {
-            int c = nb + nt * 16 + rw;
-            float bb = sb5[c];
-            float vm = 0.f;
-#pragma unroll
-            for (int m = 0; m < 4; m++)
-#pragma unroll
-                for (int r = 0; r < 4; r++) {
-                    int rr = m * 16 + kq * 4 + r;
-                    float h = relu(acc[m][nt][r] + bb);
-                    if (rr < nrows) vm = fmaxf(vm, h);
-                }
-            vm = fmaxf(vm, __shfl_xor(vm, 16));
-            vm = fmaxf(vm, __shfl_xor(vm, 32));
-            if (kq == 0) atomicMax(&netmax[b * 128 + c], __float_as_uint(vm));
-        }
+        float acc = 0.f;
+        const bf16x8* wr = (const bf16x8*)(w4t + (size_t)c * 512);
+        for (int i = 0; i < 64; i++) {
+            bf16x8 vv = wr[i];
+#pragma unroll
+            for (int j = 0; j < 8; j++) acc += h512[i * 8 + j] * bf2f((u16)vv[j]);
+        }
+        h256[c] = relu(acc + bp4[c]);
+    }
+    __syncthreads();
+    if (c < 128) {
+        float acc = 0.f;
+        const bf16x8* wr = (const bf16x8*)(w5t + (size_t)c * 256);
+        for (int i = 0; i < 32; i++) {
+            bf16x8 vv = wr[i];
+#pragma unroll
+            for (int j = 0; j < 8; j++) acc += h256[i * 8 + j] * bf2f((u16)vv[j]);
+        }
+        atomicMax(&netmax[b * 128 + c], __float_as_uint(relu(acc + bp5[c])));
     }
 }
 
@@ -513,42 +500,48 @@
                               void* d_out, int out_size, void* d_ws, size_t ws_size,
                               hipStream_t stream) {
     float* ws = (float*)d_ws;
-    u32* flag = (u32*)ws;
-
-    static const int order[28] = {0,2,3,4,5,6,7,8,9,10,11,12,13,14,15,16,17,18,19,20,21,22,23,24,25,26,27,28};
-    static const int nels[28] = {196608,192,64,256,4096,64,256,576,9,12288,128,512,32768,256,1024,1024,768,3,1536,512,2048,131072,256,1024,32768,128,512,512};
-    static const int offs[28] = {A_INPUTS,A_TC1W,A_TC1B,A_TBN1,A_TD1W,A_TD1B,A_TBN2,A_TD2W,A_TD2B,A_C1W,A_C1B,A_BN1,A_C2W,A_C2B,A_BN2,A_BN3,A_D1W,A_D1B,A_C3W,A_C3B,A_BN4,A_BLK1W,A_BLK1B,A_BLK1BN,A_BLK2W,A_BLK2B,A_BLK2BN,A_BNGF};
-    ConvArgs ca;
-    for (int i = 0; i < 28; i++) { ca.src[i] = d_in[order[i]]; ca.n[i] = nels[i]; ca.off[i] = offs[i]; }
-
     const int* indices = (const int*)d_in[1];
 
-    k_convert<<<dim3(32, 28), 256, 0, stream>>>(ca, (const u16*)d_in[4], ws, flag);
-
-    PrepArgs pa;
-    pa.src[0] = ws + A_C1W;   pa.bn[0] = ws + A_BN1;    pa.dst[0] = (u16*)(ws + T_C1WT); pa.K[0] = 96;  pa.logN[0] = 7; pa.base[0] = 0;
-    pa.src[1] = ws + A_C2W;   pa.bn[1] = ws + A_BN2;    pa.dst[1] = (u16*)(ws + T_C2WT); pa.K[1] = 128; pa.logN[1] = 8; pa.base[1] = 48;
-    pa.src[2] = ws + A_BLK1W; pa.bn[2] = ws + A_BLK1BN; pa.dst[2] = (u16*)(ws + T_W4T);  pa.K[2] = 512; pa.logN[2] = 8; pa.base[2] = 176;
-    pa.src[3] = ws + A_BLK2W; pa.bn[3] = ws + A_BLK2BN; pa.dst[3] = (u16*)(ws + T_W5T);  pa.K[3] = 256; pa.logN[3] = 7; pa.base[3] = 688;
-    k_prepw_all<<<816, 256, 0, stream>>>(pa);
-    k_prepsmall<<<1, 256, 0, stream>>>(ws);
-
-    hipMemsetAsync(ws + S_MAXF, 0, (size_t)14336 * 4, stream);
-
-    k_tnet1<<<dim3(4, 32), 256, 0, stream>>>(ws + A_INPUTS, ws + A_TC1W, ws + A_TC1B, ws + A_TBN1,
-                                             (u32*)(ws + S_XMAX));
-    k_tnet2<<<32, 64, 0, stream>>>((const float*)(ws + S_XMAX), ws + A_TD1W, ws + A_TD1B, ws + A_TBN2,
+    SmallCv sc;
+    {
+        static const int srcix[12] = {2, 3, 4, 5, 6, 7, 8, 9, 16, 17, 18, 28};
+        static const int nels[12] = {192, 64, 256, 4096, 64, 256, 576, 9, 1024, 768, 3, 512};
+        static const int offs[12] = {A_TC1W, A_TC1B, A_TBN1, A_TD1W, A_TD1B, A_TBN2, A_TD2W, A_TD2B,
+                                     A_BN3, A_D1W, A_D1B, A_BNGF};
+        for (int i = 0; i < 12; i++) { sc.src[i] = d_in[srcix[i]]; sc.n[i] = nels[i]; sc.off[i] = offs[i]; }
+    }
+    PrepWA pw;
+    pw.src[0] = d_in[10]; pw.bn[0] = d_in[12]; pw.K[0] = 96;  pw.logN[0] = 7; pw.base[0] = 0;   pw.dstoff[0] = T_C1WT;
+    pw.src[1] = d_in[13]; pw.bn[1] = d_in[15]; pw.K[1] = 128; pw.logN[1] = 8; pw.base[1] = 48;  pw.dstoff[1] = T_C2WT;
+    pw.src[2] = d_in[22]; pw.bn[2] = d_in[24]; pw.K[2] = 512; pw.logN[2] = 8; pw.base[2] = 176; pw.dstoff[2] = T_W4T;
+    pw.src[3] = d_in[25]; pw.bn[3] = d_in[27]; pw.K[3] = 256; pw.logN[3] = 7; pw.base[3] = 688; pw.dstoff[3] = T_W5T;
+    PrepSm ps;
+    ps.bn4 = d_in[21]; ps.c3w = d_in[19]; ps.c3b = d_in[20];
+    ps.bn2 = d_in[15]; ps.c2b = d_in[14];
+    ps.blk1bn = d_in[24]; ps.blk1b = d_in[23];
+    ps.bn1 = d_in[12]; ps.c1b = d_in[11];
+    ps.blk2bn = d_in[27]; ps.blk2b = d_in[26];
+
+    k_prep<<<854, 256, 0, stream>>>(sc, pw, ps, d_in[0], (const u16*)d_in[4], ws);
+
+    k_tnet<<<32, 256, 0, stream>>>(ws + A_INPUTS, ws + A_TC1W, ws + A_TC1B, ws + A_TBN1,
+                                   ws + A_TD1W, ws + A_TD1B, ws + A_TBN2,
                                    ws + A_TD2W, ws + A_TD2B, ws + S_TRF);
     k_pct<<<dim3(8, 32), 256, 0, stream>>>(ws + A_INPUTS, ws + S_TRF, ws + S_PCT);
-    k_feat<<<dim3(32, 32), 256, 0, stream>>>(ws + S_PCT, indices,
-                                             (const u16*)(ws + T_C1WT), ws + P_BP1,
-                                             (const u16*)(ws + T_C2WT), ws + P_BP2,
-                                             (u32*)(ws + S_MAXF));
-    k_gvec<<<32, 256, 0, stream>>>((u32*)(ws + S_MAXF), ws + A_BN3, ws + A_D1W, ws + A_D1B, ws + S_PCT);
-    k_mlp<<<dim3(33, 32), 256, 0, stream>>>(ws + S_PCT,
-                                            ws + P_W3S, ws + P_B3S,
-                                            (const u16*)(ws + T_W4T), ws + P_BP4,
-                                            (const u16*)(ws + T_W5T), ws + P_BP5,
-                                            (u32*)(ws + S_NETMAX));
-    k_out<<<16, 256, 0, stream>>>((u32*)(ws + S_NETMAX), ws + A_BNGF, flag, d_out);
-}
+
+    k_featmlp<<<2048, 256, 0, stream>>>(ws + S_PCT, indices,
+                                        (const u16*)(ws + T_C1WT), ws + P_BP1,
+                                        (const u16*)(ws + T_C2WT), ws + P_BP2,
+                                        (u32*)(ws + S_MAXF),
+                                        ws + P_W3S, ws + P_B3S,
+                                        (const u16*)(ws + T_W4T), ws + P_BP4,
+                                        (const u16*)(ws + T_W5T), ws + P_BP5,
+                                        (u32*)(ws + S_NETMAX));
+
+    k_gtail<<<32, 256, 0, stream>>>((u32*)(ws + S_MAXF), ws + A_BN3, ws + A_D1W, ws + A_D1B,
+                                    ws + P_W3S, ws + P_B3S,
+                                    (const u16*)(ws + T_W4T), ws + P_BP4,
+                                    (const u16*)(ws + T_W5T), ws + P_BP5,
+                                    (u32*)(ws + S_NETMAX));
+    k_out<<<16, 256, 0, stream>>>((u32*)(ws + S_NETMAX), ws + A_BNGF, (u32*)ws, d_out);
+}
```

After: 263.3 us. 1.18x slower.
